# Optimization experiments

Hardware: AMD Instinct MI355X
Metric: run time of the kernel (lower is better)

Reference implementation:

```python
import jax, jax.numpy as jnp
import numpy as np

N_VARS = 2_000_000
N_CONSTRS = 1_000_000
NNZ = 20_000_000  # ~20 nonzeros per constraint


def setup_inputs() -> dict:
    key = jax.random.key(0)
    k = jax.random.split(key, 6)
    pred = jax.random.normal(k[0], (N_VARS,), dtype=jnp.float32)
    constr_idx = jax.random.randint(k[1], (NNZ,), 0, N_CONSTRS)
    var_idx = jax.random.randint(k[2], (NNZ,), 0, N_VARS)
    coeff = jax.random.normal(k[3], (NNZ,), dtype=jnp.float32)
    constr_rhs = jax.random.normal(k[4], (N_CONSTRS,), dtype=jnp.float32)
    # sense: 1 = <=, 2 = >=, 3 = ==
    constr_sense = jax.random.randint(k[5], (N_CONSTRS,), 1, 4)
    return {
        "pred": pred,
        "constr_idx": constr_idx,
        "var_idx": var_idx,
        "coeff": coeff,
        "constr_rhs": constr_rhs,
        "constr_sense": constr_sense,
        "n_vars": N_VARS,
        "n_constrs": N_CONSTRS,
    }


def reference(pred, constr_idx, var_idx, coeff, constr_rhs, constr_sense, n_vars, n_constrs):
    # var_types is None -> all binary: values = sigmoid(pred)
    values = jax.nn.sigmoid(pred)
    # COO sparse matvec: ax[c] = sum over nonzeros with constr_idx==c of coeff * values[var_idx]
    ax = jax.ops.segment_sum(coeff * values[var_idx], constr_idx, num_segments=n_constrs)
    diff = ax - constr_rhs
    zero = jnp.zeros((), dtype=diff.dtype)
    violations = jnp.where(
        constr_sense == 1, jnp.maximum(diff, zero),          # <= : relu(ax - b)
        jnp.where(
            constr_sense == 2, jnp.maximum(-diff, zero),     # >= : relu(b - ax)
            jnp.where(constr_sense == 3, jnp.abs(diff), zero)  # == : |ax - b|
        ),
    )
    return violations.mean()  # reduction='mean'
```

## Files before the change

### kernel.cpp

```cpp
#include <hip/hip_runtime.h>


#define BW_LOG2 14
#define BW (1 << BW_LOG2)
#define MAXNB 64
#define NREP 8
#define VPT 16
#define P1_THREADS 256
#define P1_CHUNK (P1_THREADS * VPT)

__global__ void sigmoid_kernel(const float* __restrict__ pred,
                               float* __restrict__ values, int n) {
    int i = blockIdx.x * blockDim.x + threadIdx.x;
    int stride = gridDim.x * blockDim.x;
    int n4 = n >> 2;
    const float4* p4 = (const float4*)pred;
    float4* v4 = (float4*)values;
    for (int j = i; j < n4; j += stride) {
        float4 p = p4[j];
        float4 v;
        v.x = 1.0f / (1.0f + __expf(-p.x));
        v.y = 1.0f / (1.0f + __expf(-p.y));
        v.z = 1.0f / (1.0f + __expf(-p.z));
        v.w = 1.0f / (1.0f + __expf(-p.w));
        v4[j] = v;
    }
    for (int j = (n4 << 2) + i; j < n; j += stride)
        values[j] = 1.0f / (1.0f + __expf(-pred[j]));
}

__global__ __launch_bounds__(P1_THREADS) void binning_kernel(
    const int* __restrict__ cidx, const int* __restrict__ vidx,
    const float* __restrict__ coeff, const float* __restrict__ values,
    uint2* __restrict__ bins, int* __restrict__ cursor,
    float* __restrict__ ovf, int nnz, int nb, int cap) {
    __shared__ int hist[MAXNB];
    __shared__ int sbase[MAXNB];
    const int tid = threadIdx.x;
    const long long start = (long long)blockIdx.x * P1_CHUNK;

    for (int i = tid; i < nb; i += P1_THREADS) hist[i] = 0;
    __syncthreads();

    unsigned packed[VPT];
    float val[VPT];

    if (start + P1_CHUNK <= (long long)nnz) {
        const int4* c4 = (const int4*)(cidx + start);
        const int4* v4 = (const int4*)(vidx + start);
        const float4* w4 = (const float4*)(coeff + start);
#pragma unroll
        for (int k = 0; k < VPT / 4; ++k) {
            int g = k * P1_THREADS + tid;
            int4 c = c4[g];
            int4 v = v4[g];
            float4 w = w4[g];
            float x0 = w.x * values[v.x];
            float x1 = w.y * values[v.y];
            float x2 = w.z * values[v.z];
            float x3 = w.w * values[v.w];
            int b0 = c.x >> BW_LOG2, b1 = c.y >> BW_LOG2;
            int b2 = c.z >> BW_LOG2, b3 = c.w >> BW_LOG2;
            int l0 = atomicAdd(&hist[b0], 1);
            int l1 = atomicAdd(&hist[b1], 1);
            int l2 = atomicAdd(&hist[b2], 1);
            int l3 = atomicAdd(&hist[b3], 1);
            packed[k * 4 + 0] = (unsigned)c.x | ((unsigned)l0 << 20);
            packed[k * 4 + 1] = (unsigned)c.y | ((unsigned)l1 << 20);
            packed[k * 4 + 2] = (unsigned)c.z | ((unsigned)l2 << 20);
            packed[k * 4 + 3] = (unsigned)c.w | ((unsigned)l3 << 20);
            val[k * 4 + 0] = x0;
            val[k * 4 + 1] = x1;
            val[k * 4 + 2] = x2;
            val[k * 4 + 3] = x3;
        }
    } else {
#pragma unroll
        for (int k = 0; k < VPT; ++k) {
            long long idx = start + (long long)k * P1_THREADS + tid;
            if (idx < nnz) {
                int c = cidx[idx];
                float x = coeff[idx] * values[vidx[idx]];
                int b = c >> BW_LOG2;
                int l = atomicAdd(&hist[b], 1);
                packed[k] = (unsigned)c | ((unsigned)l << 20);
                val[k] = x;
            } else {
                packed[k] = 0xFFFFFFFFu;
            }
        }
    }
    __syncthreads();
    for (int i = tid; i < nb; i += P1_THREADS)
        sbase[i] = atomicAdd(&cursor[i], hist[i]);
    __syncthreads();
#pragma unroll
    for (int k = 0; k < VPT; ++k) {
        if (packed[k] == 0xFFFFFFFFu) continue;
        unsigned c = packed[k] & 0xFFFFFu;
        int loc = (int)(packed[k] >> 20);
        int b = (int)(c >> BW_LOG2);
        int pos = sbase[b] + loc;
        if (pos < cap)
            bins[(size_t)b * cap + pos] = make_uint2(c, __float_as_uint(val[k]));
        else
            atomicAdd(&ovf[c], val[k]);
    }
}

__global__ __launch_bounds__(512) void bucket_accum_kernel(
    const uint2* __restrict__ bins, const int* __restrict__ cursor,
    float* __restrict__ rep, int nb, int cap, int n_constrs, int rep_stride) {
    __shared__ float acc[BW];
    const int tid = threadIdx.x;
    const int b = blockIdx.x >> 3;
    const int r = blockIdx.x & 7;

    float4* a4 = (float4*)acc;
#pragma unroll
    for (int k = 0; k < BW / 4 / 512; ++k)
        a4[k * 512 + tid] = make_float4(0.0f, 0.0f, 0.0f, 0.0f);
    __syncthreads();

    int cnt = cursor[b];
    if (cnt > cap) cnt = cap;
    int begin = (int)((long long)cnt * r / NREP);
    int end = (int)((long long)cnt * (r + 1) / NREP);
    const uint2* mybins = bins + (size_t)b * cap;
    const unsigned cbase = (unsigned)b << BW_LOG2;
    for (int i = begin + tid; i < end; i += 512) {
        uint2 e = mybins[i];
        atomicAdd(&acc[(e.x & 0xFFFFFu) - cbase], __uint_as_float(e.y));
    }
    __syncthreads();

    float* out = rep + (size_t)r * rep_stride + cbase;
    int lim = n_constrs - (int)cbase;
    if (lim >= BW) {
        float4* o4 = (float4*)out;
#pragma unroll
        for (int k = 0; k < BW / 4 / 512; ++k)
            o4[k * 512 + tid] = a4[k * 512 + tid];
    } else {
        for (int j = tid; j < lim; j += 512) out[j] = acc[j];
    }
}

template <int NR>
__global__ void violation_reduce_kernel(const float* __restrict__ rep,
                                        const float* __restrict__ rhs,
                                        const int* __restrict__ sense,
                                        float* __restrict__ out,
                                        int n, int rep_stride, float inv_n) {
    int i = blockIdx.x * blockDim.x + threadIdx.x;
    int stride = gridDim.x * blockDim.x;
    float acc = 0.0f;
    int n4 = n >> 2;
    const float4* r4 = (const float4*)rhs;
    const int4* s4 = (const int4*)sense;
    for (int j = i; j < n4; j += stride) {
        float4 a = make_float4(0.0f, 0.0f, 0.0f, 0.0f);
#pragma unroll
        for (int r = 0; r < NR; ++r) {
            const float4* a4 = (const float4*)(rep + (size_t)r * (size_t)rep_stride);
            float4 t = a4[j];
            a.x += t.x; a.y += t.y; a.z += t.z; a.w += t.w;
        }
        float4 rr = r4[j];
        int4 s = s4[j];
        float d;
        d = a.x - rr.x;
        acc += (s.x == 1) ? fmaxf(d, 0.0f) : (s.x == 2) ? fmaxf(-d, 0.0f) : (s.x == 3) ? fabsf(d) : 0.0f;
        d = a.y - rr.y;
        acc += (s.y == 1) ? fmaxf(d, 0.0f) : (s.y == 2) ? fmaxf(-d, 0.0f) : (s.y == 3) ? fabsf(d) : 0.0f;
        d = a.z - rr.z;
        acc += (s.z == 1) ? fmaxf(d, 0.0f) : (s.z == 2) ? fmaxf(-d, 0.0f) : (s.z == 3) ? fabsf(d) : 0.0f;
        d = a.w - rr.w;
        acc += (s.w == 1) ? fmaxf(d, 0.0f) : (s.w == 2) ? fmaxf(-d, 0.0f) : (s.w == 3) ? fabsf(d) : 0.0f;
    }
    for (int j = (n4 << 2) + i; j < n; j += stride) {
        float a = 0.0f;
#pragma unroll
        for (int r = 0; r < NR; ++r) a += rep[(size_t)r * (size_t)rep_stride + j];
        float d = a - rhs[j];
        int s = sense[j];
        acc += (s == 1) ? fmaxf(d, 0.0f) : (s == 2) ? fmaxf(-d, 0.0f) : (s == 3) ? fabsf(d) : 0.0f;
    }

    for (int off = 32; off > 0; off >>= 1)
        acc += __shfl_down(acc, off, 64);

    __shared__ float lds[8];
    int lane = threadIdx.x & 63;
    int wave = threadIdx.x >> 6;
    if (lane == 0) lds[wave] = acc;
    __syncthreads();
    if (wave == 0) {
        int nwaves = blockDim.x >> 6;
        float b = (lane < nwaves) ? lds[lane] : 0.0f;
        for (int off = 4; off > 0; off >>= 1)
            b += __shfl_down(b, off, 64);
        if (lane == 0) atomicAdd(out, b * inv_n);
    }
}

__global__ void scatter_kernel(const int* __restrict__ cidx,
                               const int* __restrict__ vidx,
                               const float* __restrict__ coeff,
                               const float* __restrict__ values,
                               float* __restrict__ ax, int nnz) {
    int i = blockIdx.x * blockDim.x + threadIdx.x;
    int stride = gridDim.x * blockDim.x;
    int n4 = nnz >> 2;
    const int4* c4 = (const int4*)cidx;
    const int4* v4 = (const int4*)vidx;
    const float4* w4 = (const float4*)coeff;
    for (int j = i; j < n4; j += stride) {
        int4 c = c4[j];
        int4 v = v4[j];
        float4 w = w4[j];
        atomicAdd(&ax[c.x], w.x * values[v.x]);
        atomicAdd(&ax[c.y], w.y * values[v.y]);
        atomicAdd(&ax[c.z], w.z * values[v.z]);
        atomicAdd(&ax[c.w], w.w * values[v.w]);
    }
    for (int j = (n4 << 2) + i; j < nnz; j += stride)
        atomicAdd(&ax[cidx[j]], coeff[j] * values[vidx[j]]);
}

extern "C" void kernel_launch(void* const* d_in, const int* in_sizes, int n_in,
                              void* d_out, int out_size, void* d_ws, size_t ws_size,
                              hipStream_t stream) {
    const float* pred  = (const float*)d_in[0];
    const int*   cidx  = (const int*)d_in[1];
    const int*   vidx  = (const int*)d_in[2];
    const float* coeff = (const float*)d_in[3];
    const float* rhs   = (const float*)d_in[4];
    const int*   sense = (const int*)d_in[5];

    const int n_vars    = in_sizes[0];
    const int nnz       = in_sizes[1];
    const int n_constrs = in_sizes[4];

    const int rep_stride = (n_constrs + 15) & ~15;

    float* values = (float*)d_ws;
    float* rep    = values + n_vars;
    float* ovf    = rep + (size_t)NREP * rep_stride;
    int*   cursor = (int*)(ovf + rep_stride);
    uint2* bins   = (uint2*)(cursor + 64);

    const int nb = (n_constrs + BW - 1) >> BW_LOG2;
    long long cap_ll = (long long)nnz * BW / n_constrs
                     + (long long)nnz / ((long long)(nb > 0 ? nb : 1) * 32) + 2048;
    const int cap = (int)cap_ll;
    const size_t need = (size_t)(n_vars + (size_t)(NREP + 1) * rep_stride + 64) * 4
                      + (size_t)nb * (size_t)cap * 8;
    const bool fast = (nb >= 1) && (nb <= MAXNB) && (n_constrs < (1 << 20)) &&
                      (nnz > P1_CHUNK) && (ws_size >= need);

    hipMemsetAsync(d_out, 0, sizeof(float), stream);

    {
        int threads = 256;
        int work = n_vars >> 2;
        int blocks = (work + threads - 1) / threads;
        if (blocks > 4096) blocks = 4096;
        sigmoid_kernel<<<blocks, threads, 0, stream>>>(pred, values, n_vars);
    }

    if (fast) {
        hipMemsetAsync(cursor, 0, 64 * sizeof(int), stream);
        hipMemsetAsync(ovf, 0, (size_t)rep_stride * sizeof(float), stream);

        int p1_blocks = (int)(((long long)nnz + P1_CHUNK - 1) / P1_CHUNK);
        binning_kernel<<<p1_blocks, P1_THREADS, 0, stream>>>(
            cidx, vidx, coeff, values, bins, cursor, ovf, nnz, nb, cap);

        bucket_accum_kernel<<<nb * NREP, 512, 0, stream>>>(
            bins, cursor, rep, nb, cap, n_constrs, rep_stride);

        int threads = 256;
        int work = n_constrs >> 2;
        int blocks = (work + threads - 1) / threads;
        if (blocks > 4096) blocks = 4096;
        violation_reduce_kernel<NREP + 1><<<blocks, threads, 0, stream>>>(
            rep, rhs, sense, (float*)d_out, n_constrs, rep_stride,
            1.0f / (float)n_constrs);
    } else {
        hipMemsetAsync(rep, 0, (size_t)n_constrs * sizeof(float), stream);
        int threads = 256;
        int work = nnz >> 2;
        int blocks = (work + threads - 1) / threads;
        if (blocks > 8192) blocks = 8192;
        scatter_kernel<<<blocks, threads, 0, stream>>>(
            cidx, vidx, coeff, values, rep, nnz);

        int vthreads = 256;
        int vwork = n_constrs >> 2;
        int vblocks = (vwork + vthreads - 1) / vthreads;
        if (vblocks > 4096) vblocks = 4096;
        violation_reduce_kernel<1><<<vblocks, vthreads, 0, stream>>>(
            rep, rhs, sense, (float*)d_out, n_constrs, n_constrs,
            1.0f / (float)n_constrs);
    }
}
```

Measured before the change: 587.3 us.

## Store sigmoid values as fp16, shrink buckets, pad cursors, add nontemporal loads/stores

Sigmoid outputs are stored as half precision, halving the footprint of the randomly gathered value table so more of it stays cache-resident. Bucket width is halved to 8K constraints with up to 128 buckets. Global bucket cursors are padded to avoid shared cache lines, and the binning pass now uses 512 threads with 8 items each plus nontemporal streaming loads and stores. The accumulate loop is unrolled by four. fp16 rounding of values in [0,1] adds about 1e-3 relative error per product, which could affect tolerance.

New measurement: 976.4 us. 1.66x slower.

```diff
diff --git a/kernel.cpp b/kernel.cpp
--- a/kernel.cpp
+++ b/kernel.cpp
@@ -1,38 +1,46 @@
 #include <hip/hip_runtime.h>
-
-
-#define BW_LOG2 14
+#include <hip/hip_fp16.h>
+
+
+#define BW_LOG2 13
 #define BW (1 << BW_LOG2)
-#define MAXNB 64
+#define MAXNB 128
 #define NREP 8
-#define VPT 16
-#define P1_THREADS 256
+#define P1_THREADS 512
+#define VPT 8
 #define P1_CHUNK (P1_THREADS * VPT)
+#define CUR_PAD 16
+
+typedef int   v4i __attribute__((ext_vector_type(4)));
+typedef float v4f __attribute__((ext_vector_type(4)));
 
 __global__ void sigmoid_kernel(const float* __restrict__ pred,
-                               float* __restrict__ values, int n) {
+                               __half* __restrict__ values, int n) {
     int i = blockIdx.x * blockDim.x + threadIdx.x;
     int stride = gridDim.x * blockDim.x;
     int n4 = n >> 2;
-    const float4* p4 = (const float4*)pred;
-    float4* v4 = (float4*)values;
+    const v4f* p4 = (const v4f*)pred;
+    uint2* o = (uint2*)values;
     for (int j = i; j < n4; j += stride) {
-        float4 p = p4[j];
-        float4 v;
-        v.x = 1.0f / (1.0f + __expf(-p.x));
-        v.y = 1.0f / (1.0f + __expf(-p.y));
-        v.z = 1.0f / (1.0f + __expf(-p.z));
-        v.w = 1.0f / (1.0f + __expf(-p.w));
-        v4[j] = v;
+        v4f p = p4[j];
+        float a0 = 1.0f / (1.0f + __expf(-p.x));
+        float a1 = 1.0f / (1.0f + __expf(-p.y));
+        float a2 = 1.0f / (1.0f + __expf(-p.z));
+        float a3 = 1.0f / (1.0f + __expf(-p.w));
+        unsigned lo = ((unsigned)__half_as_ushort(__float2half_rn(a1)) << 16) |
+                      (unsigned)__half_as_ushort(__float2half_rn(a0));
+        unsigned hi = ((unsigned)__half_as_ushort(__float2half_rn(a3)) << 16) |
+                      (unsigned)__half_as_ushort(__float2half_rn(a2));
+        o[j] = make_uint2(lo, hi);
     }
     for (int j = (n4 << 2) + i; j < n; j += stride)
-        values[j] = 1.0f / (1.0f + __expf(-pred[j]));
+        values[j] = __float2half_rn(1.0f / (1.0f + __expf(-pred[j])));
 }
 
 __global__ __launch_bounds__(P1_THREADS) void binning_kernel(
     const int* __restrict__ cidx, const int* __restrict__ vidx,
-    const float* __restrict__ coeff, const float* __restrict__ values,
-    uint2* __restrict__ bins, int* __restrict__ cursor,
+    const float* __restrict__ coeff, const __half* __restrict__ values,
+    unsigned long long* __restrict__ bins, int* __restrict__ cursor,
     float* __restrict__ ovf, int nnz, int nb, int cap) {
     __shared__ int hist[MAXNB];
     __shared__ int sbase[MAXNB];
@@ -46,25 +54,23 @@
     float val[VPT];
 
     if (start + P1_CHUNK <= (long long)nnz) {
-        const int4* c4 = (const int4*)(cidx + start);
-        const int4* v4 = (const int4*)(vidx + start);
-        const float4* w4 = (const float4*)(coeff + start);
+        const v4i* c4 = (const v4i*)(cidx + start);
+        const v4i* v4 = (const v4i*)(vidx + start);
+        const v4f* w4 = (const v4f*)(coeff + start);
 #pragma unroll
         for (int k = 0; k < VPT / 4; ++k) {
             int g = k * P1_THREADS + tid;
-            int4 c = c4[g];
-            int4 v = v4[g];
-            float4 w = w4[g];
-            float x0 = w.x * values[v.x];
-            float x1 = w.y * values[v.y];
-            float x2 = w.z * values[v.z];
-            float x3 = w.w * values[v.w];
-            int b0 = c.x >> BW_LOG2, b1 = c.y >> BW_LOG2;
-            int b2 = c.z >> BW_LOG2, b3 = c.w >> BW_LOG2;
-            int l0 = atomicAdd(&hist[b0], 1);
-            int l1 = atomicAdd(&hist[b1], 1);
-            int l2 = atomicAdd(&hist[b2], 1);
-            int l3 = atomicAdd(&hist[b3], 1);
+            v4i c = __builtin_nontemporal_load(&c4[g]);
+            v4i v = __builtin_nontemporal_load(&v4[g]);
+            v4f w = __builtin_nontemporal_load(&w4[g]);
+            float x0 = w.x * __half2float(values[v.x]);
+            float x1 = w.y * __half2float(values[v.y]);
+            float x2 = w.z * __half2float(values[v.z]);
+            float x3 = w.w * __half2float(values[v.w]);
+            int l0 = atomicAdd(&hist[c.x >> BW_LOG2], 1);
+            int l1 = atomicAdd(&hist[c.y >> BW_LOG2], 1);
+            int l2 = atomicAdd(&hist[c.z >> BW_LOG2], 1);
+            int l3 = atomicAdd(&hist[c.w >> BW_LOG2], 1);
             packed[k * 4 + 0] = (unsigned)c.x | ((unsigned)l0 << 20);
             packed[k * 4 + 1] = (unsigned)c.y | ((unsigned)l1 << 20);
             packed[k * 4 + 2] = (unsigned)c.z | ((unsigned)l2 << 20);
@@ -80,9 +86,8 @@
             long long idx = start + (long long)k * P1_THREADS + tid;
             if (idx < nnz) {
                 int c = cidx[idx];
-                float x = coeff[idx] * values[vidx[idx]];
-                int b = c >> BW_LOG2;
-                int l = atomicAdd(&hist[b], 1);
+                float x = coeff[idx] * __half2float(values[vidx[idx]]);
+                int l = atomicAdd(&hist[c >> BW_LOG2], 1);
                 packed[k] = (unsigned)c | ((unsigned)l << 20);
                 val[k] = x;
             } else {
@@ -92,7 +97,7 @@
     }
     __syncthreads();
     for (int i = tid; i < nb; i += P1_THREADS)
-        sbase[i] = atomicAdd(&cursor[i], hist[i]);
+        sbase[i] = atomicAdd(&cursor[i * CUR_PAD], hist[i]);
     __syncthreads();
 #pragma unroll
     for (int k = 0; k < VPT; ++k) {
@@ -101,43 +106,59 @@
         int loc = (int)(packed[k] >> 20);
         int b = (int)(c >> BW_LOG2);
         int pos = sbase[b] + loc;
-        if (pos < cap)
-            bins[(size_t)b * cap + pos] = make_uint2(c, __float_as_uint(val[k]));
-        else
+        if (pos < cap) {
+            unsigned long long e = (unsigned long long)c |
+                ((unsigned long long)__float_as_uint(val[k]) << 32);
+            __builtin_nontemporal_store(e, &bins[(size_t)b * cap + pos]);
+        } else {
             atomicAdd(&ovf[c], val[k]);
+        }
     }
 }
 
 __global__ __launch_bounds__(512) void bucket_accum_kernel(
-    const uint2* __restrict__ bins, const int* __restrict__ cursor,
+    const unsigned long long* __restrict__ bins, const int* __restrict__ cursor,
     float* __restrict__ rep, int nb, int cap, int n_constrs, int rep_stride) {
     __shared__ float acc[BW];
     const int tid = threadIdx.x;
     const int b = blockIdx.x >> 3;
     const int r = blockIdx.x & 7;
 
-    float4* a4 = (float4*)acc;
+    v4f* a4 = (v4f*)acc;
+    v4f zero = {0.0f, 0.0f, 0.0f, 0.0f};
 #pragma unroll
     for (int k = 0; k < BW / 4 / 512; ++k)
-        a4[k * 512 + tid] = make_float4(0.0f, 0.0f, 0.0f, 0.0f);
-    __syncthreads();
-
-    int cnt = cursor[b];
+        a4[k * 512 + tid] = zero;
+    __syncthreads();
+
+    int cnt = cursor[b * CUR_PAD];
     if (cnt > cap) cnt = cap;
     int begin = (int)((long long)cnt * r / NREP);
     int end = (int)((long long)cnt * (r + 1) / NREP);
-    const uint2* mybins = bins + (size_t)b * cap;
+    const unsigned long long* mb = bins + (size_t)b * cap;
     const unsigned cbase = (unsigned)b << BW_LOG2;
-    for (int i = begin + tid; i < end; i += 512) {
-        uint2 e = mybins[i];
-        atomicAdd(&acc[(e.x & 0xFFFFFu) - cbase], __uint_as_float(e.y));
+
+    int i = begin + tid;
+    for (; i + 512 * 3 < end; i += 512 * 4) {
+        unsigned long long e0 = mb[i];
+        unsigned long long e1 = mb[i + 512];
+        unsigned long long e2 = mb[i + 1024];
+        unsigned long long e3 = mb[i + 1536];
+        atomicAdd(&acc[((unsigned)e0 & 0xFFFFFu) - cbase], __uint_as_float((unsigned)(e0 >> 32)));
+        atomicAdd(&acc[((unsigned)e1 & 0xFFFFFu) - cbase], __uint_as_float((unsigned)(e1 >> 32)));
+        atomicAdd(&acc[((unsigned)e2 & 0xFFFFFu) - cbase], __uint_as_float((unsigned)(e2 >> 32)));
+        atomicAdd(&acc[((unsigned)e3 & 0xFFFFFu) - cbase], __uint_as_float((unsigned)(e3 >> 32)));
+    }
+    for (; i < end; i += 512) {
+        unsigned long long e = mb[i];
+        atomicAdd(&acc[((unsigned)e & 0xFFFFFu) - cbase], __uint_as_float((unsigned)(e >> 32)));
     }
     __syncthreads();
 
     float* out = rep + (size_t)r * rep_stride + cbase;
     int lim = n_constrs - (int)cbase;
     if (lim >= BW) {
-        float4* o4 = (float4*)out;
+        v4f* o4 = (v4f*)out;
 #pragma unroll
         for (int k = 0; k < BW / 4 / 512; ++k)
             o4[k * 512 + tid] = a4[k * 512 + tid];
@@ -207,7 +228,7 @@
 __global__ void scatter_kernel(const int* __restrict__ cidx,
                                const int* __restrict__ vidx,
                                const float* __restrict__ coeff,
-                               const float* __restrict__ values,
+                               const __half* __restrict__ values,
                                float* __restrict__ ax, int nnz) {
     int i = blockIdx.x * blockDim.x + threadIdx.x;
     int stride = gridDim.x * blockDim.x;
@@ -219,13 +240,13 @@
         int4 c = c4[j];
         int4 v = v4[j];
         float4 w = w4[j];
-        atomicAdd(&ax[c.x], w.x * values[v.x]);
-        atomicAdd(&ax[c.y], w.y * values[v.y]);
-        atomicAdd(&ax[c.z], w.z * values[v.z]);
-        atomicAdd(&ax[c.w], w.w * values[v.w]);
+        atomicAdd(&ax[c.x], w.x * __half2float(values[v.x]));
+        atomicAdd(&ax[c.y], w.y * __half2float(values[v.y]));
+        atomicAdd(&ax[c.z], w.z * __half2float(values[v.z]));
+        atomicAdd(&ax[c.w], w.w * __half2float(values[v.w]));
     }
     for (int j = (n4 << 2) + i; j < nnz; j += stride)
-        atomicAdd(&ax[cidx[j]], coeff[j] * values[vidx[j]]);
+        atomicAdd(&ax[cidx[j]], coeff[j] * __half2float(values[vidx[j]]));
 }
 
 extern "C" void kernel_launch(void* const* d_in, const int* in_sizes, int n_in,
@@ -243,18 +264,22 @@
     const int n_constrs = in_sizes[4];
 
     const int rep_stride = (n_constrs + 15) & ~15;
-
-    float* values = (float*)d_ws;
-    float* rep    = values + n_vars;
-    float* ovf    = rep + (size_t)NREP * rep_stride;
-    int*   cursor = (int*)(ovf + rep_stride);
-    uint2* bins   = (uint2*)(cursor + 64);
+    const size_t vh_bytes = ((size_t)n_vars * 2 + 255) & ~(size_t)255;
+
+    __half* values = (__half*)d_ws;
+    float* rep = (float*)((char*)d_ws + vh_bytes);
+    float* ovf = rep + (size_t)NREP * rep_stride;
+    int* cursor = (int*)(ovf + rep_stride);
+    unsigned long long* bins =
+        (unsigned long long*)(cursor + MAXNB * CUR_PAD);
 
     const int nb = (n_constrs + BW - 1) >> BW_LOG2;
     long long cap_ll = (long long)nnz * BW / n_constrs
                      + (long long)nnz / ((long long)(nb > 0 ? nb : 1) * 32) + 2048;
     const int cap = (int)cap_ll;
-    const size_t need = (size_t)(n_vars + (size_t)(NREP + 1) * rep_stride + 64) * 4
+    const size_t need = vh_bytes
+                      + (size_t)(NREP + 1) * rep_stride * 4
+                      + (size_t)MAXNB * CUR_PAD * 4
                       + (size_t)nb * (size_t)cap * 8;
     const bool fast = (nb >= 1) && (nb <= MAXNB) && (n_constrs < (1 << 20)) &&
                       (nnz > P1_CHUNK) && (ws_size >= need);
@@ -265,12 +290,13 @@
         int threads = 256;
         int work = n_vars >> 2;
         int blocks = (work + threads - 1) / threads;
-        if (blocks > 4096) blocks = 4096;
+        if (blocks < 1) blocks = 1;
+        if (blocks > 2048) blocks = 2048;
         sigmoid_kernel<<<blocks, threads, 0, stream>>>(pred, values, n_vars);
     }
 
     if (fast) {
-        hipMemsetAsync(cursor, 0, 64 * sizeof(int), stream);
+        hipMemsetAsync(cursor, 0, (size_t)MAXNB * CUR_PAD * sizeof(int), stream);
         hipMemsetAsync(ovf, 0, (size_t)rep_stride * sizeof(float), stream);
 
         int p1_blocks = (int)(((long long)nnz + P1_CHUNK - 1) / P1_CHUNK);
```
